# Performance work log

Measured on AMD Instinct MI355X. Metric: run time of the kernel, lower is better.

The kernel has to match this reference:

```python
import jax, jax.numpy as jnp
import numpy as np

NEG_SLOPE = 0.2

def gat_conv(x, src, dst, n_nodes, W, a_src, a_dst, bias, heads, out_ch, concat):
    # Linear transform per head: (N, H, C)
    h = (x @ W).reshape(n_nodes, heads, out_ch)
    # Per-node attention logits (N, H)
    al_src = jnp.sum(h * a_src, axis=-1)
    al_dst = jnp.sum(h * a_dst, axis=-1)
    # Per-edge score with LeakyReLU (E, H)
    e = jax.nn.leaky_relu(al_src[src] + al_dst[dst], NEG_SLOPE)
    # Segment softmax over incoming edges of each dst node
    m = jax.ops.segment_max(e, dst, num_segments=n_nodes)
    e = jnp.exp(e - jax.lax.stop_gradient(m)[dst])
    denom = jax.ops.segment_sum(e, dst, num_segments=n_nodes)
    alpha = e / denom[dst]                      # (E, H)
    # Weighted scatter-aggregate of source features
    msg = h[src] * alpha[:, :, None]            # (E, H, C)
    out = jax.ops.segment_sum(msg, dst, num_segments=n_nodes)  # (N, H, C)
    out = out.reshape(n_nodes, heads * out_ch) if concat else out.mean(axis=1)
    return out + bias


def setup_inputs() -> dict:
    key = jax.random.key(0)
    ks = jax.random.split(key, 12)
    N, E = 100000, 1600000
    IN, HID, OUT, H1 = 256, 128, 4, 2
    x = jax.random.normal(ks[0], (N, IN), dtype=jnp.float32)
    edge_index = jax.random.randint(ks[1], (2, E), 0, N, dtype=jnp.int64)
    s = 1.0 / np.sqrt(IN)
    W1 = jax.random.uniform(ks[2], (IN, H1 * HID), jnp.float32, -s, s)
    a_src1 = jax.random.uniform(ks[3], (H1, HID), jnp.float32, -s, s)
    a_dst1 = jax.random.uniform(ks[4], (H1, HID), jnp.float32, -s, s)
    b1 = jnp.zeros((H1 * HID,), jnp.float32)
    s2 = 1.0 / np.sqrt(H1 * HID)
    W2 = jax.random.uniform(ks[5], (H1 * HID, OUT), jnp.float32, -s2, s2)
    a_src2 = jax.random.uniform(ks[6], (1, OUT), jnp.float32, -s2, s2)
    a_dst2 = jax.random.uniform(ks[7], (1, OUT), jnp.float32, -s2, s2)
    b2 = jnp.zeros((OUT,), jnp.float32)
    return {"x": x, "edge_index": edge_index, "W1": W1, "a_src1": a_src1,
            "a_dst1": a_dst1, "b1": b1, "W2": W2, "a_src2": a_src2,
            "a_dst2": a_dst2, "b2": b2}


def reference(x, edge_index, W1, a_src1, a_dst1, b1, W2, a_src2, a_dst2, b2):
    N = x.shape[0]
    # PyG GATConv default: add self-loops
    loop = jnp.arange(N, dtype=edge_index.dtype)
    src = jnp.concatenate([edge_index[0], loop])
    dst = jnp.concatenate([edge_index[1], loop])
    h = gat_conv(x, src, dst, N, W1, a_src1, a_dst1, b1, heads=2, out_ch=128, concat=True)
    h = jax.nn.relu(h)
    # dropout p=0.4 skipped (eval mode)
    out = gat_conv(h, src, dst, N, W2, a_src2, a_dst2, b2, heads=1, out_ch=4, concat=False)
    return jax.nn.log_softmax(out, axis=1)
```

## Files before the change

kernel.cpp:

```cpp
#include <hip/hip_runtime.h>
#include <hip/hip_bf16.h>

#define NEG_SLOPE 0.2f
#define SCAN_TPB 256
#define SCAN_VPT 4
#define SCAN_ELEMS (SCAN_TPB * SCAN_VPT)

typedef __attribute__((ext_vector_type(8))) short short8;
typedef __attribute__((ext_vector_type(4))) float f32x4;

static __device__ __forceinline__ unsigned short f2bf(float v) {
    __hip_bfloat16 b = __float2bfloat16(v);
    return *reinterpret_cast<unsigned short*>(&b);
}
static __device__ __forceinline__ float bf2f(unsigned short u) {
    unsigned int x = ((unsigned int)u) << 16;
    return __uint_as_float(x);
}
static __device__ __forceinline__ float lrelu(float v) {
    return (v > 0.f) ? v : NEG_SLOPE * v;
}


__global__ void hist_kernel(const int* __restrict__ dst_idx, int* __restrict__ count,
                            int E, int N) {
    int e = blockIdx.x * blockDim.x + threadIdx.x;
    int EN = E + N;
    if (e >= EN) return;
    int d = (e < E) ? dst_idx[e] : (e - E);
    atomicAdd(&count[d], 1);
}

__global__ void scan_blocks_kernel(const int* __restrict__ count, int* __restrict__ local_ex,
                                   int* __restrict__ blockSums, int n) {
    __shared__ int sm[SCAN_TPB];
    int tid = threadIdx.x;
    int base = blockIdx.x * SCAN_ELEMS + tid * SCAN_VPT;
    int v[SCAN_VPT];
    int s = 0;
#pragma unroll
    for (int i = 0; i < SCAN_VPT; i++) {
        v[i] = (base + i < n) ? count[base + i] : 0;
        s += v[i];
    }
    sm[tid] = s;
    __syncthreads();
#pragma unroll
    for (int off = 1; off < SCAN_TPB; off <<= 1) {
        int t = (tid >= off) ? sm[tid - off] : 0;
        __syncthreads();
        sm[tid] += t;
        __syncthreads();
    }
    int ex = sm[tid] - s;
#pragma unroll
    for (int i = 0; i < SCAN_VPT; i++) {
        if (base + i < n) local_ex[base + i] = ex;
        ex += v[i];
    }
    if (tid == SCAN_TPB - 1) blockSums[blockIdx.x] = sm[tid];
}

__global__ void scan_sums_kernel(int* __restrict__ blockSums, int nb) {
    __shared__ int sm[128];
    int tid = threadIdx.x;
    int v = (tid < nb) ? blockSums[tid] : 0;
    sm[tid] = v;
    __syncthreads();
    for (int off = 1; off < 128; off <<= 1) {
        int t = (tid >= off) ? sm[tid - off] : 0;
        __syncthreads();
        sm[tid] += t;
        __syncthreads();
    }
    if (tid < nb) blockSums[tid] = sm[tid] - v;
}

__global__ void scan_finalize_kernel(int* __restrict__ offsets, const int* __restrict__ blockSums,
                                     int* __restrict__ cursor, int n, int total) {
    int tid = threadIdx.x;
    int base = blockIdx.x * SCAN_ELEMS + tid * SCAN_VPT;
    int add = blockSums[blockIdx.x];
#pragma unroll
    for (int i = 0; i < SCAN_VPT; i++) {
        int idx = base + i;
        if (idx < n) {
            int val = offsets[idx] + add;
            offsets[idx] = val;
            cursor[idx] = val;
        }
    }
    if (blockIdx.x == 0 && tid == 0) offsets[n] = total;
}

__global__ void scatter_kernel(const int* __restrict__ src_idx, const int* __restrict__ dst_idx,
                               int* __restrict__ cursor, int* __restrict__ csr_src,
                               int E, int N) {
    int e = blockIdx.x * blockDim.x + threadIdx.x;
    int EN = E + N;
    if (e >= EN) return;
    int s, d;
    if (e < E) {
        s = src_idx[e];
        d = dst_idx[e];
    } else {
        s = d = e - E;
    }
    int pos = atomicAdd(&cursor[d], 1);
    csr_src[pos] = s;
}


__global__ __launch_bounds__(256) void prep_xs(const float* __restrict__ x,
                                               unsigned short* __restrict__ xs, int total8) {
    int i = blockIdx.x * 256 + threadIdx.x;
    if (i >= total8) return;
    float4 v0 = *reinterpret_cast<const float4*>(x + (size_t)i * 8);
    float4 v1 = *reinterpret_cast<const float4*>(x + (size_t)i * 8 + 4);
    ushort4 u0, u1;
    u0.x = f2bf(v0.x); u0.y = f2bf(v0.y); u0.z = f2bf(v0.z); u0.w = f2bf(v0.w);
    u1.x = f2bf(v1.x); u1.y = f2bf(v1.y); u1.z = f2bf(v1.z); u1.w = f2bf(v1.w);
    *reinterpret_cast<ushort4*>(xs + (size_t)i * 8) = u0;
    *reinterpret_cast<ushort4*>(xs + (size_t)i * 8 + 4) = u1;
}


__global__ __launch_bounds__(256) void prep_w1s(const float* __restrict__ W1,
                                                unsigned short* __restrict__ W1s) {
    int idx = blockIdx.x * 256 + threadIdx.x;
    int col = idx & 255;
    int k = idx >> 8;
    int t = k >> 5, lg = (k >> 3) & 3, kk = k & 7;
    int j = col >> 4, lc = col & 15;
    W1s[t * 8192 + lg * 2048 + lc * 128 + j * 8 + kk] = f2bf(W1[k * 256 + col]);
}


__global__ __launch_bounds__(256, 4) void gemm1_kernel(
    const unsigned short* __restrict__ xs, const unsigned short* __restrict__ W1s,
    const float* __restrict__ a_src1, const float* __restrict__ a_dst1,
    unsigned short* __restrict__ h1, float* __restrict__ al_src1,
    float* __restrict__ al_dst1, int N) {
    const int tid = threadIdx.x;
    const int w = tid >> 6, l = tid & 63;
    const int lc = l & 15, lg = l >> 4;

    const int arow = blockIdx.x * 64 + w * 16 + lc;
    const int arowc = (arow < N) ? arow : (N - 1);

    const unsigned short* xp = xs + (size_t)arowc * 256 + lg * 8;
    short8 af[8];
#pragma unroll
    for (int t = 0; t < 8; t++) af[t] = *reinterpret_cast<const short8*>(xp + t * 32);

    f32x4 acc[16];
#pragma unroll
    for (int j = 0; j < 16; j++) acc[j] = (f32x4){0.f, 0.f, 0.f, 0.f};

    const unsigned short* wbase = W1s + lg * 2048 + lc * 128;
#pragma unroll
    for (int t = 0; t < 8; t++) {
        const unsigned short* wp = wbase + t * 8192;
#pragma unroll
        for (int j = 0; j < 16; j++) {
            short8 bf = *reinterpret_cast<const short8*>(wp + j * 8);
            acc[j] = __builtin_amdgcn_mfma_f32_16x16x32_bf16(af[t], bf, acc[j], 0, 0, 0);
        }
    }

    const int rbase = blockIdx.x * 64 + w * 16 + lg * 4;

#pragma unroll
    for (int j = 0; j < 16; j++) {
#pragma unroll
        for (int r = 0; r < 4; r++) {
            int rr = rbase + r;
            if (rr < N) h1[(size_t)rr * 256 + j * 16 + lc] = f2bf(acc[j][r]);
        }
    }

    float as_[16], ad_[16];
#pragma unroll
    for (int j = 0; j < 16; j++) {
        as_[j] = a_src1[j * 16 + lc];
        ad_[j] = a_dst1[j * 16 + lc];
    }
#pragma unroll
    for (int r = 0; r < 4; r++) {
        float s0 = 0.f, d0 = 0.f, s1 = 0.f, d1 = 0.f;
#pragma unroll
        for (int j = 0; j < 8; j++) {
            s0 += acc[j][r] * as_[j];
            d0 += acc[j][r] * ad_[j];
        }
#pragma unroll
        for (int j = 8; j < 16; j++) {
            s1 += acc[j][r] * as_[j];
            d1 += acc[j][r] * ad_[j];
        }
#pragma unroll
        for (int mask = 8; mask >= 1; mask >>= 1) {
            s0 += __shfl_xor(s0, mask, 64);
            s1 += __shfl_xor(s1, mask, 64);
            d0 += __shfl_xor(d0, mask, 64);
            d1 += __shfl_xor(d1, mask, 64);
        }
        int rr = rbase + r;
        if (lc == 0 && rr < N) {
            al_src1[rr * 2 + 0] = s0;
            al_src1[rr * 2 + 1] = s1;
            al_dst1[rr * 2 + 0] = d0;
            al_dst1[rr * 2 + 1] = d1;
        }
    }
}


__global__ __launch_bounds__(256) void agg1_kernel(
    const unsigned short* __restrict__ h1,
    const float* __restrict__ al_src1, const float* __restrict__ al_dst1,
    const int* __restrict__ offsets, const int* __restrict__ csr_src,
    const float* __restrict__ b1, const float* __restrict__ W2,
    const float* __restrict__ a_src2, const float* __restrict__ a_dst2,
    float* __restrict__ g2out, float* __restrict__ al_src2o,
    float* __restrict__ al_dst2o, int N) {
    int wid = (blockIdx.x * blockDim.x + threadIdx.x) >> 6;
    if (wid >= N) return;
    int lane = threadIdx.x & 63;
    int head = lane >> 5;
    int ch = lane * 4;

    int beg = offsets[wid], end = offsets[wid + 1];
    float aldv = al_dst1[wid * 2 + head];

    float l = 0.f, p0 = 0.f, p1 = 0.f, p2 = 0.f, p3 = 0.f;

    int e = beg;
    for (; e + 3 < end; e += 4) {
        int sa = csr_src[e];
        int sb = csr_src[e + 1];
        int sc = csr_src[e + 2];
        int sd = csr_src[e + 3];
        float la = al_src1[sa * 2 + head] + aldv;
        float lb = al_src1[sb * 2 + head] + aldv;
        float lcv = al_src1[sc * 2 + head] + aldv;
        float ld = al_src1[sd * 2 + head] + aldv;
        ushort4 ha = *reinterpret_cast<const ushort4*>(h1 + (size_t)sa * 256 + ch);
        ushort4 hb = *reinterpret_cast<const ushort4*>(h1 + (size_t)sb * 256 + ch);
        ushort4 hc = *reinterpret_cast<const ushort4*>(h1 + (size_t)sc * 256 + ch);
        ushort4 hd = *reinterpret_cast<const ushort4*>(h1 + (size_t)sd * 256 + ch);
        float wa = __expf(lrelu(la));
        float wb = __expf(lrelu(lb));
        float wc = __expf(lrelu(lcv));
        float wd = __expf(lrelu(ld));
        p0 += wa * bf2f(ha.x) + wb * bf2f(hb.x) + wc * bf2f(hc.x) + wd * bf2f(hd.x);
        p1 += wa * bf2f(ha.y) + wb * bf2f(hb.y) + wc * bf2f(hc.y) + wd * bf2f(hd.y);
        p2 += wa * bf2f(ha.z) + wb * bf2f(hb.z) + wc * bf2f(hc.z) + wd * bf2f(hd.z);
        p3 += wa * bf2f(ha.w) + wb * bf2f(hb.w) + wc * bf2f(hc.w) + wd * bf2f(hd.w);
        l += (wa + wb) + (wc + wd);
    }
    for (; e < end; ++e) {
        int sa = csr_src[e];
        float la = al_src1[sa * 2 + head] + aldv;
        ushort4 ha = *reinterpret_cast<const ushort4*>(h1 + (size_t)sa * 256 + ch);
        float wa = __expf(lrelu(la));
        p0 += wa * bf2f(ha.x);
        p1 += wa * bf2f(ha.y);
        p2 += wa * bf2f(ha.z);
        p3 += wa * bf2f(ha.w);
        l += wa;
    }

    float inv = 1.f / l;
    float4 bb = *reinterpret_cast<const float4*>(b1 + ch);
    float r0 = fmaxf(p0 * inv + bb.x, 0.f);
    float r1 = fmaxf(p1 * inv + bb.y, 0.f);
    float r2 = fmaxf(p2 * inv + bb.z, 0.f);
    float r3 = fmaxf(p3 * inv + bb.w, 0.f);

    float4 w0 = *reinterpret_cast<const float4*>(W2 + (size_t)(ch + 0) * 4);
    float4 w1 = *reinterpret_cast<const float4*>(W2 + (size_t)(ch + 1) * 4);
    float4 w2 = *reinterpret_cast<const float4*>(W2 + (size_t)(ch + 2) * 4);
    float4 w3 = *reinterpret_cast<const float4*>(W2 + (size_t)(ch + 3) * 4);
    float g0 = r0 * w0.x + r1 * w1.x + r2 * w2.x + r3 * w3.x;
    float g1 = r0 * w0.y + r1 * w1.y + r2 * w2.y + r3 * w3.y;
    float g2v = r0 * w0.z + r1 * w1.z + r2 * w2.z + r3 * w3.z;
    float g3 = r0 * w0.w + r1 * w1.w + r2 * w2.w + r3 * w3.w;
#pragma unroll
    for (int mask = 32; mask >= 1; mask >>= 1) {
        g0 += __shfl_xor(g0, mask, 64);
        g1 += __shfl_xor(g1, mask, 64);
        g2v += __shfl_xor(g2v, mask, 64);
        g3 += __shfl_xor(g3, mask, 64);
    }
    if (lane == 0) {
        float4 gv;
        gv.x = g0; gv.y = g1; gv.z = g2v; gv.w = g3;
        *reinterpret_cast<float4*>(g2out + (size_t)wid * 4) = gv;
        al_src2o[wid] = g0 * a_src2[0] + g1 * a_src2[1] + g2v * a_src2[2] + g3 * a_src2[3];
        al_dst2o[wid] = g0 * a_dst2[0] + g1 * a_dst2[1] + g2v * a_dst2[2] + g3 * a_dst2[3];
    }
}


__global__ __launch_bounds__(256) void agg2_kernel(
    const float* __restrict__ g2, const float* __restrict__ al_src2,
    const float* __restrict__ al_dst2, const int* __restrict__ offsets,
    const int* __restrict__ csr_src, const float* __restrict__ b2,
    float* __restrict__ out, int N) {
    int nid = blockIdx.x * 256 + threadIdx.x;
    if (nid >= N) return;

    int beg = offsets[nid], end = offsets[nid + 1];
    float aldv = al_dst2[nid];

    float l = 0.f, p0 = 0.f, p1 = 0.f, p2 = 0.f, p3 = 0.f;

    int e = beg;
    for (; e + 3 < end; e += 4) {
        int sa = csr_src[e];
        int sb = csr_src[e + 1];
        int sc = csr_src[e + 2];
        int sd = csr_src[e + 3];
        float la = al_src2[sa] + aldv;
        float lb = al_src2[sb] + aldv;
        float lcv = al_src2[sc] + aldv;
        float ld = al_src2[sd] + aldv;
        float4 ga = *reinterpret_cast<const float4*>(g2 + (size_t)sa * 4);
        float4 gb = *reinterpret_cast<const float4*>(g2 + (size_t)sb * 4);
        float4 gc = *reinterpret_cast<const float4*>(g2 + (size_t)sc * 4);
        float4 gd = *reinterpret_cast<const float4*>(g2 + (size_t)sd * 4);
        float wa = __expf(lrelu(la));
        float wb = __expf(lrelu(lb));
        float wc = __expf(lrelu(lcv));
        float wd = __expf(lrelu(ld));
        p0 += wa * ga.x + wb * gb.x + wc * gc.x + wd * gd.x;
        p1 += wa * ga.y + wb * gb.y + wc * gc.y + wd * gd.y;
        p2 += wa * ga.z + wb * gb.z + wc * gc.z + wd * gd.z;
        p3 += wa * ga.w + wb * gb.w + wc * gc.w + wd * gd.w;
        l += (wa + wb) + (wc + wd);
    }
    for (; e < end; ++e) {
        int sa = csr_src[e];
        float la = al_src2[sa] + aldv;
        float4 ga = *reinterpret_cast<const float4*>(g2 + (size_t)sa * 4);
        float wa = __expf(lrelu(la));
        p0 += wa * ga.x;
        p1 += wa * ga.y;
        p2 += wa * ga.z;
        p3 += wa * ga.w;
        l += wa;
    }

    float inv = 1.f / l;
    float r0 = p0 * inv + b2[0];
    float r1 = p1 * inv + b2[1];
    float r2 = p2 * inv + b2[2];
    float r3 = p3 * inv + b2[3];
    float mx = fmaxf(fmaxf(r0, r1), fmaxf(r2, r3));
    float s0 = __expf(r0 - mx), s1 = __expf(r1 - mx), s2 = __expf(r2 - mx), s3 = __expf(r3 - mx);
    float ls = __logf(s0 + s1 + s2 + s3);
    float4 ov;
    ov.x = r0 - mx - ls;
    ov.y = r1 - mx - ls;
    ov.z = r2 - mx - ls;
    ov.w = r3 - mx - ls;
    *reinterpret_cast<float4*>(out + (size_t)nid * 4) = ov;
}


extern "C" void kernel_launch(void* const* d_in, const int* in_sizes, int n_in,
                              void* d_out, int out_size, void* d_ws, size_t ws_size,
                              hipStream_t stream) {
    const float* x = (const float*)d_in[0];
    const int* edge_index = (const int*)d_in[1];
    const float* W1 = (const float*)d_in[2];
    const float* a_src1 = (const float*)d_in[3];
    const float* a_dst1 = (const float*)d_in[4];
    const float* b1 = (const float*)d_in[5];
    const float* W2 = (const float*)d_in[6];
    const float* a_src2 = (const float*)d_in[7];
    const float* a_dst2 = (const float*)d_in[8];
    const float* b2 = (const float*)d_in[9];
    float* out = (float*)d_out;

    const int N = in_sizes[0] / 256;
    const int E = in_sizes[1] / 2;
    const int EN = E + N;
    const int* src_idx = edge_index;
    const int* dst_idx = edge_index + E;

    char* ws = (char*)d_ws;
    size_t off = 0;
    auto alloc = [&](size_t bytes) -> char* {
        char* p = ws + off;
        off += (bytes + 255) & ~(size_t)255;
        return p;
    };
    unsigned short* h1 = (unsigned short*)alloc((size_t)N * 256 * 2);
    unsigned short* xs = (unsigned short*)alloc((size_t)N * 256 * 2);
    unsigned short* W1s = (unsigned short*)alloc((size_t)256 * 256 * 2);
    float* al_src1 = (float*)alloc((size_t)N * 2 * 4);
    float* al_dst1 = (float*)alloc((size_t)N * 2 * 4);
    float* g2 = (float*)alloc((size_t)N * 4 * 4);
    float* al_src2 = (float*)alloc((size_t)N * 4);
    float* al_dst2 = (float*)alloc((size_t)N * 4);
    int* offsets = (int*)alloc((size_t)(N + 1) * 4);
    int* cursor = (int*)alloc((size_t)N * 4);
    int* csr_src = (int*)alloc((size_t)EN * 4);
    int* blockSums = (int*)alloc(128 * 4);

    hipMemsetAsync(cursor, 0, (size_t)N * 4, stream);

    prep_w1s<<<256, 256, 0, stream>>>(W1, W1s);
    int total8 = N * 32;
    prep_xs<<<(total8 + 255) / 256, 256, 0, stream>>>(x, xs, total8);

    int hb = (EN + 255) / 256;
    hist_kernel<<<hb, 256, 0, stream>>>(dst_idx, cursor, E, N);

    int nb = (N + SCAN_ELEMS - 1) / SCAN_ELEMS;
    scan_blocks_kernel<<<nb, SCAN_TPB, 0, stream>>>(cursor, offsets, blockSums, N);
    scan_sums_kernel<<<1, 128, 0, stream>>>(blockSums, nb);
    scan_finalize_kernel<<<nb, SCAN_TPB, 0, stream>>>(offsets, blockSums, cursor, N, EN);

    scatter_kernel<<<hb, 256, 0, stream>>>(src_idx, dst_idx, cursor, csr_src, E, N);

    int gb = (N + 63) / 64;
    gemm1_kernel<<<gb, 256, 0, stream>>>(xs, W1s, a_src1, a_dst1, h1, al_src1, al_dst1, N);

    int ab = (N + 3) / 4;
    agg1_kernel<<<ab, 256, 0, stream>>>(h1, al_src1, al_dst1, offsets, csr_src, b1, W2,
                                        a_src2, a_dst2, g2, al_src2, al_dst2, N);
    agg2_kernel<<<(N + 255) / 256, 256, 0, stream>>>(g2, al_src2, al_dst2, offsets, csr_src,
                                                     b2, out, N);
}
```

Before: 627.2 us.

## Two-pass bucketed CSR build and split GEMM1 columns across blocks

Replaces the single random-scatter CSR build with two passes. First, edges are binned into 512-node buckets using shared-memory counters and one global atomic per bucket. Then a per-bucket pass places each edge with localized atomics, so atomics and writes stay within a small address window. Separately, GEMM1 is split so each block computes half of the 256 output columns, doubling the grid and halving accumulator registers. The cost is an extra 8-byte-per-edge pair buffer pass and A-tile loads done twice.

After: 590.0 us. 5.9% less time.

```diff
diff --git a/kernel.cpp b/kernel.cpp
--- a/kernel.cpp
+++ b/kernel.cpp
@@ -5,6 +5,7 @@
 #define SCAN_TPB 256
 #define SCAN_VPT 4
 #define SCAN_ELEMS (SCAN_TPB * SCAN_VPT)
+#define BIN_CHUNK 2048
 
 typedef __attribute__((ext_vector_type(8))) short short8;
 typedef __attribute__((ext_vector_type(4))) float f32x4;
@@ -93,21 +94,75 @@
     if (blockIdx.x == 0 && tid == 0) offsets[n] = total;
 }
 
-__global__ void scatter_kernel(const int* __restrict__ src_idx, const int* __restrict__ dst_idx,
-                               int* __restrict__ cursor, int* __restrict__ csr_src,
-                               int E, int N) {
-    int e = blockIdx.x * blockDim.x + threadIdx.x;
-    int EN = E + N;
-    if (e >= EN) return;
-    int s, d;
-    if (e < E) {
-        s = src_idx[e];
-        d = dst_idx[e];
-    } else {
-        s = d = e - E;
-    }
-    int pos = atomicAdd(&cursor[d], 1);
-    csr_src[pos] = s;
+
+__global__ void bucket_init_kernel(const int* __restrict__ offsets, int* __restrict__ bucketCursor,
+                                   int nbuck, int N) {
+    int tid = threadIdx.x;
+    if (tid < nbuck) bucketCursor[tid] = offsets[tid << 9];
+}
+
+__global__ __launch_bounds__(256) void bin_kernel(const int* __restrict__ src_idx,
+                                                  const int* __restrict__ dst_idx,
+                                                  int* __restrict__ bucketCursor,
+                                                  int2* __restrict__ pairbuf, int E, int N) {
+    __shared__ int cnt[256];
+    __shared__ int gbase[256];
+    const int tid = threadIdx.x;
+    const int EN = E + N;
+    const int nbuck = (N + 511) >> 9;
+
+    cnt[tid] = 0;
+    __syncthreads();
+
+    int e0 = blockIdx.x * BIN_CHUNK + tid * 8;
+    int sv[8], dv[8], bk[8], rk[8];
+#pragma unroll
+    for (int i = 0; i < 8; i++) {
+        int e = e0 + i;
+        if (e < EN) {
+            int s, d;
+            if (e < E) {
+                s = src_idx[e];
+                d = dst_idx[e];
+            } else {
+                s = d = e - E;
+            }
+            sv[i] = s;
+            dv[i] = d;
+            bk[i] = d >> 9;
+            rk[i] = atomicAdd(&cnt[bk[i]], 1);
+        } else {
+            bk[i] = -1;
+        }
+    }
+    __syncthreads();
+    if (tid < nbuck && cnt[tid] > 0) gbase[tid] = atomicAdd(&bucketCursor[tid], cnt[tid]);
+    __syncthreads();
+#pragma unroll
+    for (int i = 0; i < 8; i++) {
+        if (bk[i] >= 0) {
+            int2 p;
+            p.x = sv[i];
+            p.y = dv[i];
+            pairbuf[gbase[bk[i]] + rk[i]] = p;
+        }
+    }
+}
+
+__global__ __launch_bounds__(256) void sortb_kernel(const int2* __restrict__ pairbuf,
+                                                    const int* __restrict__ offsets,
+                                                    int* __restrict__ cursor,
+                                                    int* __restrict__ csr_src, int N) {
+    int b = blockIdx.x;
+    int nodeEnd = (b + 1) << 9;
+    if (nodeEnd > N) nodeEnd = N;
+    int pBeg = offsets[b << 9];
+    int pEnd = offsets[nodeEnd];
+    for (int i = pBeg + threadIdx.x; i < pEnd; i += 256) {
+        int2 p = pairbuf[i];
+        int pos = atomicAdd(&cursor[p.y], 1);
+        csr_src[pos] = p.x;
+    }
 }
 
 
@@ -144,8 +199,9 @@
     const int tid = threadIdx.x;
     const int w = tid >> 6, l = tid & 63;
     const int lc = l & 15, lg = l >> 4;
-
-    const int arow = blockIdx.x * 64 + w * 16 + lc;
+    const int rb = blockIdx.x >> 1, jh = blockIdx.x & 1;
+
+    const int arow = rb * 64 + w * 16 + lc;
     const int arowc = (arow < N) ? arow : (N - 1);
 
     const unsigned short* xp = xs + (size_t)arowc * 256 + lg * 8;
@@ -153,64 +209,55 @@
 #pragma unroll
     for (int t = 0; t < 8; t++) af[t] = *reinterpret_cast<const short8*>(xp + t * 32);
 
-    f32x4 acc[16];
-#pragma unroll
-    for (int j = 0; j < 16; j++) acc[j] = (f32x4){0.f, 0.f, 0.f, 0.f};
-
-    const unsigned short* wbase = W1s + lg * 2048 + lc * 128;
+    f32x4 acc[8];
+#pragma unroll
+    for (int j = 0; j < 8; j++) acc[j] = (f32x4){0.f, 0.f, 0.f, 0.f};
+
+    const unsigned short* wbase = W1s + lg * 2048 + lc * 128 + jh * 64;
 #pragma unroll
     for (int t = 0; t < 8; t++) {
         const unsigned short* wp = wbase + t * 8192;
 #pragma unroll
-        for (int j = 0; j < 16; j++) {
+        for (int j = 0; j < 8; j++) {
             short8 bf = *reinterpret_cast<const short8*>(wp + j * 8);
             acc[j] = __builtin_amdgcn_mfma_f32_16x16x32_bf16(af[t], bf, acc[j], 0, 0, 0);
         }
     }
 
-    const int rbase = blockIdx.x * 64 + w * 16 + lg * 4;
-
-#pragma unroll
-    for (int j = 0; j < 16; j++) {
+    const int rbase = rb * 64 + w * 16 + lg * 4;
+
+#pragma unroll
+    for (int j = 0; j < 8; j++) {
 #pragma unroll
         for (int r = 0; r < 4; r++) {
             int rr = rbase + r;
-            if (rr < N) h1[(size_t)rr * 256 + j * 16 + lc] = f2bf(acc[j][r]);
-        }
-    }
-
-    float as_[16], ad_[16];
-#pragma unroll
-    for (int j = 0; j < 16; j++) {
-        as_[j] = a_src1[j * 16 + lc];
-        ad_[j] = a_dst1[j * 16 + lc];
+            if (rr < N) h1[(size_t)rr * 256 + jh * 128 + j * 16 + lc] = f2bf(acc[j][r]);
+        }
+    }
+
+    float as_[8], ad_[8];
+#pragma unroll
+    for (int j = 0; j < 8; j++) {
+        as_[j] = a_src1[jh * 128 + j * 16 + lc];
+        ad_[j] = a_dst1[jh * 128 + j * 16 + lc];
     }
 #pragma unroll
     for (int r = 0; r < 4; r++) {
-        float s0 = 0.f, d0 = 0.f, s1 = 0.f, d1 = 0.f;
+        float s0 = 0.f, d0 = 0.f;
 #pragma unroll
         for (int j = 0; j < 8; j++) {
             s0 += acc[j][r] * as_[j];
             d0 += acc[j][r] * ad_[j];
         }
 #pragma unroll
-        for (int j = 8; j < 16; j++) {
-            s1 += acc[j][r] * as_[j];
-            d1 += acc[j][r] * ad_[j];
-        }
-#pragma unroll
         for (int mask = 8; mask >= 1; mask >>= 1) {
             s0 += __shfl_xor(s0, mask, 64);
-            s1 += __shfl_xor(s1, mask, 64);
             d0 += __shfl_xor(d0, mask, 64);
-            d1 += __shfl_xor(d1, mask, 64);
         }
         int rr = rbase + r;
         if (lc == 0 && rr < N) {
-            al_src1[rr * 2 + 0] = s0;
-            al_src1[rr * 2 + 1] = s1;
-            al_dst1[rr * 2 + 0] = d0;
-            al_dst1[rr * 2 + 1] = d1;
+            al_src1[rr * 2 + jh] = s0;
+            al_dst1[rr * 2 + jh] = d0;
         }
     }
 }
@@ -408,6 +455,8 @@
     int* offsets = (int*)alloc((size_t)(N + 1) * 4);
     int* cursor = (int*)alloc((size_t)N * 4);
     int* csr_src = (int*)alloc((size_t)EN * 4);
+    int2* pairbuf = (int2*)alloc((size_t)EN * 8);
+    int* bucketCursor = (int*)alloc(256 * 4);
     int* blockSums = (int*)alloc(128 * 4);
 
     hipMemsetAsync(cursor, 0, (size_t)N * 4, stream);
@@ -424,9 +473,13 @@
     scan_sums_kernel<<<1, 128, 0, stream>>>(blockSums, nb);
     scan_finalize_kernel<<<nb, SCAN_TPB, 0, stream>>>(offsets, blockSums, cursor, N, EN);
 
-    scatter_kernel<<<hb, 256, 0, stream>>>(src_idx, dst_idx, cursor, csr_src, E, N);
-
-    int gb = (N + 63) / 64;
+    int nbuck = (N + 511) >> 9;
+    bucket_init_kernel<<<1, 256, 0, stream>>>(offsets, bucketCursor, nbuck, N);
+    int binb = (EN + BIN_CHUNK - 1) / BIN_CHUNK;
+    bin_kernel<<<binb, 256, 0, stream>>>(src_idx, dst_idx, bucketCursor, pairbuf, E, N);
+    sortb_kernel<<<nbuck, 256, 0, stream>>>(pairbuf, offsets, cursor, csr_src, N);
+
+    int gb = ((N + 63) / 64) * 2;
     gemm1_kernel<<<gb, 256, 0, stream>>>(xs, W1s, a_src1, a_dst1, h1, al_src1, al_dst1, N);
 
     int ab = (N + 3) / 4;
```
